# Optimization experiments

Measured on AMD Instinct MI355X. Metric: run time of the kernel, lower is better.

## Reference

```python
import jax, jax.numpy as jnp
import numpy as np

EMBED_DIM = 768
NUM_HEADS = 12
HEAD_DIM = EMBED_DIM // NUM_HEADS
SCALE = HEAD_DIM ** -0.5


def setup_inputs() -> dict:
    key = jax.random.key(0)
    ks = jax.random.split(key, 5)
    B, N, D = 2, 4096, EMBED_DIM
    std = 1.0 / np.sqrt(D)
    x = jax.random.normal(ks[0], (B, N, D), dtype=jnp.float32)
    W_qkv = jax.random.normal(ks[1], (D, 3 * D), dtype=jnp.float32) * std
    b_qkv = jax.random.normal(ks[2], (3 * D,), dtype=jnp.float32) * 0.01
    W_proj = jax.random.normal(ks[3], (D, D), dtype=jnp.float32) * std
    b_proj = jax.random.normal(ks[4], (D,), dtype=jnp.float32) * 0.01
    return {"x": x, "W_qkv": W_qkv, "b_qkv": b_qkv, "W_proj": W_proj, "b_proj": b_proj}


def reference(x, W_qkv, b_qkv, W_proj, b_proj):
    B, N, D = x.shape
    H, Hd = NUM_HEADS, HEAD_DIM
    qkv = x @ W_qkv + b_qkv                      # [B, N, 3D]
    qkv = qkv.reshape(B, N, 3, H, Hd)
    qkv = jnp.transpose(qkv, (2, 0, 3, 1, 4))    # [3, B, H, N, Hd]
    q, k, v = qkv[0], qkv[1], qkv[2]
    attn = jnp.einsum('bhqd,bhkd->bhqk', q, k) * SCALE   # [B, H, N, N]
    attn = jax.nn.softmax(attn, axis=-1)
    out = jnp.einsum('bhqk,bhkd->bhqd', attn, v)          # [B, H, N, Hd]
    out = jnp.transpose(out, (0, 2, 1, 3)).reshape(B, N, D)
    return out @ W_proj + b_proj
```

## Files before the change

### kernel.cpp

```cpp
#include <hip/hip_runtime.h>
#include <hip/hip_bf16.h>

typedef __attribute__((ext_vector_type(4))) float f32x4;
typedef __attribute__((ext_vector_type(16))) float f32x16;
typedef __attribute__((ext_vector_type(8))) short s16x8;
typedef __attribute__((ext_vector_type(4))) unsigned int u32x4;

#define MFMA16(a, b, c) __builtin_amdgcn_mfma_f32_16x16x32_bf16(a, b, c, 0, 0, 0)
#define MFMA32(a, b, c) __builtin_amdgcn_mfma_f32_32x32x16_bf16(a, b, c, 0, 0, 0)

__device__ __forceinline__ short f2bf(float f) {
  unsigned u = __builtin_bit_cast(unsigned, f);
  u += 0x7fffu + ((u >> 16) & 1u);
  return (short)(u >> 16);
}
__device__ __forceinline__ unsigned cvtpk(float lo, float hi) {
  unsigned r;
  asm("v_cvt_pk_bf16_f32 %0, %1, %2" : "=v"(r) : "v"(lo), "v"(hi));
  return r;
}
__device__ __forceinline__ float ex2(float x) {
  float r;
  asm("v_exp_f32 %0, %1" : "=v"(r) : "v"(x));
  return r;
}
__device__ __forceinline__ void vperm(const s16x8 a, const s16x8 b,
                                      s16x8& w0, s16x8& w1) {
#pragma unroll
  for (int e = 0; e < 4; ++e) {
    w0[e] = a[e];
    w0[4 + e] = b[e];
    w1[e] = a[4 + e];
    w1[4 + e] = b[4 + e];
  }
}
__device__ __forceinline__ void gl_lds16(const unsigned short* g, short* l) {
  __builtin_amdgcn_global_load_lds(
      (const __attribute__((address_space(1))) unsigned int*)g,
      (__attribute__((address_space(3))) unsigned int*)l, 16, 0, 0);
}

__global__ __launch_bounds__(256) void convert_x(
    const float* __restrict__ X, unsigned short* __restrict__ Xb) {
  const size_t i = ((size_t)blockIdx.x * 256 + threadIdx.x) * 8;
  f32x4 a = *(const f32x4*)(X + i);
  f32x4 b = *(const f32x4*)(X + i + 4);
  s16x8 o;
#pragma unroll
  for (int e = 0; e < 4; ++e) o[e] = f2bf(a[e]);
#pragma unroll
  for (int e = 0; e < 4; ++e) o[4 + e] = f2bf(b[e]);
  *(s16x8*)(Xb + i) = o;
}

__global__ __launch_bounds__(256) void tconv(
    const float* __restrict__ W, unsigned short* __restrict__ Wt,
    int K, int N) {
  __shared__ float T[64][65];
  const int k0 = blockIdx.x * 64, n0 = blockIdx.y * 64;
  const int t = threadIdx.x;
  const int tr = t >> 4, tc = (t & 15) * 4;
#pragma unroll
  for (int i = 0; i < 4; ++i) {
    f32x4 v = *(const f32x4*)&W[(size_t)(k0 + tr + i * 16) * N + n0 + tc];
#pragma unroll
    for (int e = 0; e < 4; ++e) T[tc + e][tr + i * 16] = v[e];
  }
  __syncthreads();
  const int nn = t >> 2, kk = (t & 3) * 16;
  s16x8 o0, o1;
#pragma unroll
  for (int j = 0; j < 8; ++j) o0[j] = f2bf(T[nn][kk + j]);
#pragma unroll
  for (int j = 0; j < 8; ++j) o1[j] = f2bf(T[nn][kk + 8 + j]);
  *(s16x8*)&Wt[(size_t)(n0 + nn) * K + k0 + kk] = o0;
  *(s16x8*)&Wt[(size_t)(n0 + nn) * K + k0 + kk + 8] = o1;
}

__global__ __launch_bounds__(256) void qkv_gemm(
    const unsigned short* __restrict__ Xb, const unsigned short* __restrict__ Wt,
    const float* __restrict__ bias, unsigned short* __restrict__ Qo,
    unsigned short* __restrict__ Ko, unsigned short* __restrict__ VTo) {
  __shared__ __align__(16) short As[128 * 32];
  __shared__ __align__(16) short Bs[128 * 32];
  const int m0 = blockIdx.x * 128, n0 = blockIdx.y * 128;
  const int tid = threadIdx.x, lane = tid & 63, wid = tid >> 6;
  const int wr = wid >> 1, wc = wid & 1;
  const int lr = lane & 15, s4 = lane >> 4;

  const int crow = lane >> 2;
  const int ccol = (lane & 3) ^ (crow & 3);
  const unsigned short* ga0 = Xb + (size_t)(m0 + wid * 32 + crow) * 768 + ccol * 8;
  const unsigned short* ga1 = ga0 + (size_t)16 * 768;
  const unsigned short* gb0 = Wt + (size_t)(n0 + wid * 32 + crow) * 768 + ccol * 8;
  const unsigned short* gb1 = gb0 + (size_t)16 * 768;
  short* lA0 = &As[(wid * 2) * 512];
  short* lA1 = &As[(wid * 2 + 1) * 512];
  short* lB0 = &Bs[(wid * 2) * 512];
  short* lB1 = &Bs[(wid * 2 + 1) * 512];

  f32x4 acc[4][4];
#pragma unroll
  for (int i = 0; i < 4; ++i)
#pragma unroll
    for (int j = 0; j < 4; ++j)
#pragma unroll
      for (int e = 0; e < 4; ++e) acc[i][j][e] = 0.f;

  for (int k0 = 0; k0 < 768; k0 += 32) {
    gl_lds16(ga0 + k0, lA0);
    gl_lds16(ga1 + k0, lA1);
    gl_lds16(gb0 + k0, lB0);
    gl_lds16(gb1 + k0, lB1);
    __syncthreads();
    s16x8 af[4], bfr[4];
#pragma unroll
    for (int mi = 0; mi < 4; ++mi) {
      const int row = wr * 64 + mi * 16 + lr;
      af[mi] = *(const s16x8*)&As[row * 32 + ((s4 ^ (row & 3)) << 3)];
    }
#pragma unroll
    for (int ni = 0; ni < 4; ++ni) {
      const int row = wc * 64 + ni * 16 + lr;
      bfr[ni] = *(const s16x8*)&Bs[row * 32 + ((s4 ^ (row & 3)) << 3)];
    }
#pragma unroll
    for (int mi = 0; mi < 4; ++mi)
#pragma unroll
      for (int ni = 0; ni < 4; ++ni)
        acc[mi][ni] = MFMA16(af[mi], bfr[ni], acc[mi][ni]);
    __syncthreads();
  }

  const float QSC = 0.18033688011f;
  const int rbase = m0 + wr * 64 + (lane >> 4) * 4;
#pragma unroll
  for (int ni = 0; ni < 4; ++ni) {
    const int cb = n0 + wc * 64 + ni * 16;
    const int which = cb / 768;
    const int rem = cb - which * 768;
    const int h = rem >> 6;
    const int d = (rem & 63) + lr;
    const float bi = bias[cb + lr];
#pragma unroll
    for (int mi = 0; mi < 4; ++mi) {
#pragma unroll
      for (int j = 0; j < 4; ++j) {
        const int row = rbase + mi * 16 + j;
        const int bb = row >> 12, t = row & 4095;
        const float v = acc[mi][ni][j] + bi;
        const size_t hb = (size_t)(bb * 12 + h);
        if (which == 0)
          Qo[(hb * 4096 + t) * 64 + d] = (unsigned short)f2bf(v * QSC);
        else if (which == 1)
          Ko[(hb * 4096 + t) * 64 + d] = (unsigned short)f2bf(v);
        else
          VTo[(hb * 64 + d) * 4096 + t] = (unsigned short)f2bf(v);
      }
    }
  }
}

__global__ __launch_bounds__(256) void attn_fwd(
    const unsigned short* __restrict__ Qg, const unsigned short* __restrict__ Kg,
    const unsigned short* __restrict__ VTg, unsigned short* __restrict__ Aout) {
  __shared__ __align__(16) short smem[16384];
  const int qt = blockIdx.x, bh = blockIdx.y;
  const unsigned short* Qh = Qg + (size_t)bh * 4096 * 64;
  const unsigned short* Kh = Kg + (size_t)bh * 4096 * 64;
  const unsigned short* Vh = VTg + (size_t)bh * 4096 * 64;
  const int tid = threadIdx.x, lane = tid & 63, wid = tid >> 6;
  const int l31 = lane & 31, hi = lane >> 5;
  const int sw0 = (l31 + (l31 >> 3)) & 7;
  const int sw1 = (sw0 + 4) & 7;
  const int qbase = qt * 128 + wid * 32;

  s16x8 qf[4];
#pragma unroll
  for (int db = 0; db < 4; ++db)
    qf[db] = *(const s16x8*)&Qh[(size_t)(qbase + l31) * 64 + db * 16 + hi * 8];

  s16x8 ones;
#pragma unroll
  for (int e = 0; e < 8; ++e) ones[e] = (short)0x3F80;

  f32x16 zf;
#pragma unroll
  for (int r = 0; r < 16; ++r) zf[r] = 0.f;
  f32x16 o0 = zf, o1 = zf, accl = zf;

  const int srow = tid >> 2, sp = tid & 3;
  const int ssw = (srow + (srow >> 3)) & 7;
  const int sd0 = srow * 64 + (((sp * 2) ^ ssw) << 3);
  const int sd1 = srow * 64 + (((sp * 2 + 1) ^ ssw) << 3);
  const unsigned short* kga = Kh + srow * 64 + sp * 16;
  const unsigned short* vga = Vh + (size_t)srow * 4096 + sp * 16;

  s16x8 kr0 = *(const s16x8*)kga;
  s16x8 kr1 = *(const s16x8*)(kga + 8);
  s16x8 vr0 = *(const s16x8*)vga;
  s16x8 vr1 = *(const s16x8*)(vga + 8);
  {
    s16x8 w0, w1;
    vperm(vr0, vr1, w0, w1);
    *(s16x8*)&smem[sd0] = kr0;
    *(s16x8*)&smem[sd1] = kr1;
    *(s16x8*)&smem[8192 + sd0] = w0;
    *(s16x8*)&smem[8192 + sd1] = w1;
  }
  __syncthreads();

  int cur = 0;
  for (int t = 0; t < 64; ++t) {
    if (t < 63) {
      kr0 = *(const s16x8*)(kga + (size_t)(t + 1) * 4096);
      kr1 = *(const s16x8*)(kga + (size_t)(t + 1) * 4096 + 8);
      vr0 = *(const s16x8*)(vga + (t + 1) * 64);
      vr1 = *(const s16x8*)(vga + (t + 1) * 64 + 8);
    }
    const short* Kc = smem + cur * 4096;
    const short* Vc = smem + 8192 + cur * 4096;

    f32x16 sA = zf, sB = zf;
    __builtin_amdgcn_s_setprio(1);
#pragma unroll
    for (int db = 0; db < 4; ++db) {
      s16x8 kf = *(const s16x8*)&Kc[l31 * 64 + (((db * 2 + hi) ^ sw0) << 3)];
      sA = MFMA32(kf, qf[db], sA);
    }
#pragma unroll
    for (int db = 0; db < 4; ++db) {
      s16x8 kf = *(const s16x8*)&Kc[(32 + l31) * 64 + (((db * 2 + hi) ^ sw1) << 3)];
      sB = MFMA32(kf, qf[db], sB);
    }
    __builtin_amdgcn_s_setprio(0);

#pragma unroll
    for (int r = 0; r < 16; ++r) {
      sA[r] = ex2(sA[r]);
      sB[r] = ex2(sB[r]);
    }
    s16x8 pf0, pf1, pf2, pf3;
#define PACK_PF(pfv, sv, bse)                                           \
  {                                                                     \
    u32x4 fw;                                                           \
    fw[0] = cvtpk(sv[bse + 0], sv[bse + 1]);                            \
    fw[1] = cvtpk(sv[bse + 2], sv[bse + 3]);                            \
    fw[2] = cvtpk(sv[bse + 4], sv[bse + 5]);                            \
    fw[3] = cvtpk(sv[bse + 6], sv[bse + 7]);                            \
    pfv = __builtin_bit_cast(s16x8, fw);                                \
  }
    PACK_PF(pf0, sA, 0)
    PACK_PF(pf1, sA, 8)
    PACK_PF(pf2, sB, 0)
    PACK_PF(pf3, sB, 8)
#undef PACK_PF

    __builtin_amdgcn_s_setprio(1);
    accl = MFMA32(ones, pf0, accl);
    accl = MFMA32(ones, pf1, accl);
    accl = MFMA32(ones, pf2, accl);
    accl = MFMA32(ones, pf3, accl);

    {
      const short* Vr = &Vc[l31 * 64];
      s16x8 v0 = *(const s16x8*)&Vr[((0 + hi) ^ sw0) << 3];
      o0 = MFMA32(v0, pf0, o0);
      s16x8 v1 = *(const s16x8*)&Vr[((2 + hi) ^ sw0) << 3];
      o0 = MFMA32(v1, pf1, o0);
      s16x8 v2 = *(const s16x8*)&Vr[((4 + hi) ^ sw0) << 3];
      o0 = MFMA32(v2, pf2, o0);
      s16x8 v3 = *(const s16x8*)&Vr[((6 + hi) ^ sw0) << 3];
      o0 = MFMA32(v3, pf3, o0);
      const short* Vr1 = &Vc[(32 + l31) * 64];
      s16x8 w0 = *(const s16x8*)&Vr1[((0 + hi) ^ sw1) << 3];
      o1 = MFMA32(w0, pf0, o1);
      s16x8 w1 = *(const s16x8*)&Vr1[((2 + hi) ^ sw1) << 3];
      o1 = MFMA32(w1, pf1, o1);
      s16x8 w2 = *(const s16x8*)&Vr1[((4 + hi) ^ sw1) << 3];
      o1 = MFMA32(w2, pf2, o1);
      s16x8 w3 = *(const s16x8*)&Vr1[((6 + hi) ^ sw1) << 3];
      o1 = MFMA32(w3, pf3, o1);
    }
    __builtin_amdgcn_s_setprio(0);

    if (t < 63) {
      const int nb = cur ^ 1;
      s16x8 w0, w1;
      vperm(vr0, vr1, w0, w1);
      *(s16x8*)&smem[nb * 4096 + sd0] = kr0;
      *(s16x8*)&smem[nb * 4096 + sd1] = kr1;
      *(s16x8*)&smem[8192 + nb * 4096 + sd0] = w0;
      *(s16x8*)&smem[8192 + nb * 4096 + sd1] = w1;
      __syncthreads();
      cur = nb;
    }
  }

  __syncthreads();
  short* Ow = smem + wid * (32 * 72);
  const float inv = 1.0f / accl[0];
#pragma unroll
  for (int r = 0; r < 16; ++r) {
    const int dd = (r & 3) + 8 * (r >> 2) + 4 * hi;
    Ow[l31 * 72 + dd] = f2bf(o0[r] * inv);
    Ow[l31 * 72 + 32 + dd] = f2bf(o1[r] * inv);
  }
  const int b = bh / 12, h = bh - b * 12;
  const int qq = lane >> 1, c0 = (lane & 1) * 32;
  const size_t gb = ((size_t)(b * 4096 + qbase + qq)) * 768 + h * 64 + c0;
#pragma unroll
  for (int i = 0; i < 4; ++i) {
    s16x8 v = *(const s16x8*)&Ow[qq * 72 + c0 + i * 8];
    *(s16x8*)&Aout[gb + i * 8] = v;
  }
}

__global__ __launch_bounds__(256) void proj_gemm(
    const unsigned short* __restrict__ A, const unsigned short* __restrict__ Wt,
    const float* __restrict__ bias, float* __restrict__ out) {
  __shared__ __align__(16) short As[128 * 32];
  __shared__ __align__(16) short Bs[128 * 32];
  const int m0 = blockIdx.x * 128, n0 = blockIdx.y * 128;
  const int tid = threadIdx.x, lane = tid & 63, wid = tid >> 6;
  const int wr = wid >> 1, wc = wid & 1;
  const int lr = lane & 15, s4 = lane >> 4;

  const int crow = lane >> 2;
  const int ccol = (lane & 3) ^ (crow & 3);
  const unsigned short* ga0 = A + (size_t)(m0 + wid * 32 + crow) * 768 + ccol * 8;
  const unsigned short* ga1 = ga0 + (size_t)16 * 768;
  const unsigned short* gb0 = Wt + (size_t)(n0 + wid * 32 + crow) * 768 + ccol * 8;
  const unsigned short* gb1 = gb0 + (size_t)16 * 768;
  short* lA0 = &As[(wid * 2) * 512];
  short* lA1 = &As[(wid * 2 + 1) * 512];
  short* lB0 = &Bs[(wid * 2) * 512];
  short* lB1 = &Bs[(wid * 2 + 1) * 512];

  f32x4 acc[4][4];
#pragma unroll
  for (int i = 0; i < 4; ++i)
#pragma unroll
    for (int j = 0; j < 4; ++j)
#pragma unroll
      for (int e = 0; e < 4; ++e) acc[i][j][e] = 0.f;

  for (int k0 = 0; k0 < 768; k0 += 32) {
    gl_lds16(ga0 + k0, lA0);
    gl_lds16(ga1 + k0, lA1);
    gl_lds16(gb0 + k0, lB0);
    gl_lds16(gb1 + k0, lB1);
    __syncthreads();
    s16x8 af[4], bfr[4];
#pragma unroll
    for (int mi = 0; mi < 4; ++mi) {
      const int row = wr * 64 + mi * 16 + lr;
      af[mi] = *(const s16x8*)&As[row * 32 + ((s4 ^ (row & 3)) << 3)];
    }
#pragma unroll
    for (int ni = 0; ni < 4; ++ni) {
      const int row = wc * 64 + ni * 16 + lr;
      bfr[ni] = *(const s16x8*)&Bs[row * 32 + ((s4 ^ (row & 3)) << 3)];
    }
#pragma unroll
    for (int mi = 0; mi < 4; ++mi)
#pragma unroll
      for (int ni = 0; ni < 4; ++ni)
        acc[mi][ni] = MFMA16(af[mi], bfr[ni], acc[mi][ni]);
    __syncthreads();
  }

  const int rbase = m0 + wr * 64 + (lane >> 4) * 4;
#pragma unroll
  for (int ni = 0; ni < 4; ++ni) {
    const int cb = n0 + wc * 64 + ni * 16;
    const float bi = bias[cb + lr];
#pragma unroll
    for (int mi = 0; mi < 4; ++mi) {
#pragma unroll
      for (int j = 0; j < 4; ++j) {
        const int row = rbase + mi * 16 + j;
        out[(size_t)row * 768 + cb + lr] = acc[mi][ni][j] + bi;
      }
    }
  }
}

extern "C" void kernel_launch(void* const* d_in, const int* in_sizes, int n_in,
                              void* d_out, int out_size, void* d_ws, size_t ws_size,
                              hipStream_t stream) {
  const float* x = (const float*)d_in[0];
  const float* W_qkv = (const float*)d_in[1];
  const float* b_qkv = (const float*)d_in[2];
  const float* W_proj = (const float*)d_in[3];
  const float* b_proj = (const float*)d_in[4];
  float* out = (float*)d_out;

  unsigned short* ws = (unsigned short*)d_ws;
  const size_t NQ = (size_t)24 * 4096 * 64;
  unsigned short* q = ws;
  unsigned short* k = ws + NQ;
  unsigned short* vt = ws + 2 * NQ;
  unsigned short* xb_attn = ws + 3 * NQ;
  unsigned short* wqt = ws + 4 * NQ;
  unsigned short* wpt = wqt + (size_t)2304 * 768;

  convert_x<<<3072, 256, 0, stream>>>(x, xb_attn);
  tconv<<<dim3(12, 36), 256, 0, stream>>>(W_qkv, wqt, 768, 2304);
  tconv<<<dim3(12, 12), 256, 0, stream>>>(W_proj, wpt, 768, 768);
  qkv_gemm<<<dim3(64, 18), 256, 0, stream>>>(xb_attn, wqt, b_qkv, q, k, vt);
  attn_fwd<<<dim3(32, 24), 256, 0, stream>>>(q, k, vt, xb_attn);
  proj_gemm<<<dim3(64, 6), 256, 0, stream>>>(xb_attn, wpt, b_proj, out);
}
```

Measured before the change: 233.3 us.

## Split attention KV range in two and combine partial outputs

```diff
diff --git a/kernel.cpp b/kernel.cpp
--- a/kernel.cpp
+++ b/kernel.cpp
@@ -161,11 +161,15 @@
   }
 }
 
+template <int NSPLIT>
 __global__ __launch_bounds__(256) void attn_fwd(
     const unsigned short* __restrict__ Qg, const unsigned short* __restrict__ Kg,
-    const unsigned short* __restrict__ VTg, unsigned short* __restrict__ Aout) {
+    const unsigned short* __restrict__ VTg, unsigned short* __restrict__ Aout,
+    float* __restrict__ Opart, float* __restrict__ Lpart) {
+  constexpr int TKV = 64 / NSPLIT;
   __shared__ __align__(16) short smem[16384];
-  const int qt = blockIdx.x, bh = blockIdx.y;
+  const int qt = blockIdx.x, bh = blockIdx.y, sz = blockIdx.z;
+  const int tok0 = sz * TKV * 64;
   const unsigned short* Qh = Qg + (size_t)bh * 4096 * 64;
   const unsigned short* Kh = Kg + (size_t)bh * 4096 * 64;
   const unsigned short* Vh = VTg + (size_t)bh * 4096 * 64;
@@ -193,8 +197,8 @@
   const int ssw = (srow + (srow >> 3)) & 7;
   const int sd0 = srow * 64 + (((sp * 2) ^ ssw) << 3);
   const int sd1 = srow * 64 + (((sp * 2 + 1) ^ ssw) << 3);
-  const unsigned short* kga = Kh + srow * 64 + sp * 16;
-  const unsigned short* vga = Vh + (size_t)srow * 4096 + sp * 16;
+  const unsigned short* kga = Kh + (size_t)(tok0 + srow) * 64 + sp * 16;
+  const unsigned short* vga = Vh + (size_t)srow * 4096 + tok0 + sp * 16;
 
   s16x8 kr0 = *(const s16x8*)kga;
   s16x8 kr1 = *(const s16x8*)(kga + 8);
@@ -211,8 +215,8 @@
   __syncthreads();
 
   int cur = 0;
-  for (int t = 0; t < 64; ++t) {
-    if (t < 63) {
+  for (int t = 0; t < TKV; ++t) {
+    if (t < TKV - 1) {
       kr0 = *(const s16x8*)(kga + (size_t)(t + 1) * 4096);
       kr1 = *(const s16x8*)(kga + (size_t)(t + 1) * 4096 + 8);
       vr0 = *(const s16x8*)(vga + (t + 1) * 64);
@@ -284,7 +288,7 @@
     }
     __builtin_amdgcn_s_setprio(0);
 
-    if (t < 63) {
+    if (t < TKV - 1) {
       const int nb = cur ^ 1;
       s16x8 w0, w1;
       vperm(vr0, vr1, w0, w1);
@@ -297,23 +301,67 @@
     }
   }
 
+  if constexpr (NSPLIT == 1) {
+    __syncthreads();
+    short* Ow = smem + wid * (32 * 72);
+    const float inv = 1.0f / accl[0];
+#pragma unroll
+    for (int r = 0; r < 16; ++r) {
+      const int dd = (r & 3) + 8 * (r >> 2) + 4 * hi;
+      Ow[l31 * 72 + dd] = f2bf(o0[r] * inv);
+      Ow[l31 * 72 + 32 + dd] = f2bf(o1[r] * inv);
+    }
+    const int b = bh / 12, h = bh - b * 12;
+    const int qq = lane >> 1, c0 = (lane & 1) * 32;
+    const size_t gb = ((size_t)(b * 4096 + qbase + qq)) * 768 + h * 64 + c0;
+#pragma unroll
+    for (int i = 0; i < 4; ++i) {
+      s16x8 v = *(const s16x8*)&Ow[qq * 72 + c0 + i * 8];
+      *(s16x8*)&Aout[gb + i * 8] = v;
+    }
+  } else {
+    const int q = qbase + l31;
+    const size_t ob = ((size_t)(sz * 24 + bh)) * 64 * 4096;
+#pragma unroll
+    for (int r = 0; r < 16; ++r) {
+      const int dd = (r & 3) + 8 * (r >> 2) + 4 * hi;
+      Opart[ob + (size_t)dd * 4096 + q] = o0[r];
+      Opart[ob + (size_t)(dd + 32) * 4096 + q] = o1[r];
+    }
+    Lpart[(size_t)(sz * 24 + bh) * 4096 + q] = accl[0];
+  }
+}
+
+__global__ __launch_bounds__(256) void attn_combine(
+    const float* __restrict__ Opart, const float* __restrict__ Lpart,
+    unsigned short* __restrict__ Aout) {
+  __shared__ float T[64][65];
+  const int q0 = blockIdx.x * 64, bh = blockIdx.y;
+  const int t = threadIdx.x;
+  const int d = t >> 2, qc = (t & 3) * 16;
+  const size_t b0 = ((size_t)bh * 64 + d) * 4096 + q0 + qc;
+  const size_t b1 = ((size_t)(24 + bh) * 64 + d) * 4096 + q0 + qc;
+#pragma unroll
+  for (int i = 0; i < 4; ++i) {
+    f32x4 v = *(const f32x4*)&Opart[b0 + i * 4];
+    f32x4 w = *(const f32x4*)&Opart[b1 + i * 4];
+#pragma unroll
+    for (int e = 0; e < 4; ++e) T[qc + i * 4 + e][d] = v[e] + w[e];
+  }
   __syncthreads();
-  short* Ow = smem + wid * (32 * 72);
-  const float inv = 1.0f / accl[0];
-#pragma unroll
-  for (int r = 0; r < 16; ++r) {
-    const int dd = (r & 3) + 8 * (r >> 2) + 4 * hi;
-    Ow[l31 * 72 + dd] = f2bf(o0[r] * inv);
-    Ow[l31 * 72 + 32 + dd] = f2bf(o1[r] * inv);
-  }
+  const int q = t >> 2, dc = (t & 3) * 16;
+  const float l = Lpart[(size_t)bh * 4096 + q0 + q] +
+                  Lpart[(size_t)(24 + bh) * 4096 + q0 + q];
+  const float inv = 1.0f / l;
   const int b = bh / 12, h = bh - b * 12;
-  const int qq = lane >> 1, c0 = (lane & 1) * 32;
-  const size_t gb = ((size_t)(b * 4096 + qbase + qq)) * 768 + h * 64 + c0;
-#pragma unroll
-  for (int i = 0; i < 4; ++i) {
-    s16x8 v = *(const s16x8*)&Ow[qq * 72 + c0 + i * 8];
-    *(s16x8*)&Aout[gb + i * 8] = v;
-  }
+  s16x8 o0, o1;
+#pragma unroll
+  for (int e = 0; e < 8; ++e) o0[e] = f2bf(T[q][dc + e] * inv);
+#pragma unroll
+  for (int e = 0; e < 8; ++e) o1[e] = f2bf(T[q][dc + 8 + e] * inv);
+  const size_t gb = ((size_t)(b * 4096 + q0 + q)) * 768 + h * 64 + dc;
+  *(s16x8*)&Aout[gb] = o0;
+  *(s16x8*)&Aout[gb + 8] = o1;
 }
 
 __global__ __launch_bounds__(256) void proj_gemm(
@@ -405,10 +453,22 @@
   unsigned short* wqt = ws + 4 * NQ;
   unsigned short* wpt = wqt + (size_t)2304 * 768;
 
+  const size_t base_bytes = (4 * NQ + (size_t)2304 * 768 + (size_t)768 * 768) * 2;
+  const size_t opart_bytes = (size_t)2 * 24 * 64 * 4096 * 4;
+  const size_t lpart_bytes = (size_t)2 * 24 * 4096 * 4;
+  const bool split = ws_size >= base_bytes + opart_bytes + lpart_bytes;
+  float* Opart = (float*)((char*)d_ws + base_bytes);
+  float* Lpart = (float*)((char*)d_ws + base_bytes + opart_bytes);
+
   convert_x<<<3072, 256, 0, stream>>>(x, xb_attn);
   tconv<<<dim3(12, 36), 256, 0, stream>>>(W_qkv, wqt, 768, 2304);
   tconv<<<dim3(12, 12), 256, 0, stream>>>(W_proj, wpt, 768, 768);
   qkv_gemm<<<dim3(64, 18), 256, 0, stream>>>(xb_attn, wqt, b_qkv, q, k, vt);
-  attn_fwd<<<dim3(32, 24), 256, 0, stream>>>(q, k, vt, xb_attn);
+  if (split) {
+    attn_fwd<2><<<dim3(32, 24, 2), 256, 0, stream>>>(q, k, vt, xb_attn, Opart, Lpart);
+    attn_combine<<<dim3(64, 24), 256, 0, stream>>>(Opart, Lpart, xb_attn);
+  } else {
+    attn_fwd<1><<<dim3(32, 24, 1), 256, 0, stream>>>(q, k, vt, xb_attn, Opart, Lpart);
+  }
   proj_gemm<<<dim3(64, 6), 256, 0, stream>>>(xb_attn, wpt, b_proj, out);
 }
```

After: 242.2 us. 3.8% more time.

## Load K/V tiles directly to LDS and pre-permute V^T in QKV epilogue

Applied to the files above, without the earlier changes.

```diff
diff --git a/kernel.cpp b/kernel.cpp
--- a/kernel.cpp
+++ b/kernel.cpp
@@ -23,16 +23,6 @@
   float r;
   asm("v_exp_f32 %0, %1" : "=v"(r) : "v"(x));
   return r;
-}
-__device__ __forceinline__ void vperm(const s16x8 a, const s16x8 b,
-                                      s16x8& w0, s16x8& w1) {
-#pragma unroll
-  for (int e = 0; e < 4; ++e) {
-    w0[e] = a[e];
-    w0[4 + e] = b[e];
-    w1[e] = a[4 + e];
-    w1[4 + e] = b[4 + e];
-  }
 }
 __device__ __forceinline__ void gl_lds16(const unsigned short* g, short* l) {
   __builtin_amdgcn_global_load_lds(
@@ -133,7 +123,9 @@
   }
 
   const float QSC = 0.18033688011f;
-  const int rbase = m0 + wr * 64 + (lane >> 4) * 4;
+  const int lg = lane >> 4;
+  const int plg = ((lg & 1) << 1) | ((lg >> 1) & 1);
+  const int rbase = m0 + wr * 64 + lg * 4;
 #pragma unroll
   for (int ni = 0; ni < 4; ++ni) {
     const int cb = n0 + wc * 64 + ni * 16;
@@ -154,8 +146,10 @@
           Qo[(hb * 4096 + t) * 64 + d] = (unsigned short)f2bf(v * QSC);
         else if (which == 1)
           Ko[(hb * 4096 + t) * 64 + d] = (unsigned short)f2bf(v);
-        else
-          VTo[(hb * 64 + d) * 4096 + t] = (unsigned short)f2bf(v);
+        else {
+          const int tp = (t & ~15) + plg * 4 + j;
+          VTo[(hb * 64 + d) * 4096 + tp] = (unsigned short)f2bf(v);
+        }
       }
     }
   }
@@ -189,34 +183,34 @@
   for (int r = 0; r < 16; ++r) zf[r] = 0.f;
   f32x16 o0 = zf, o1 = zf, accl = zf;
 
-  const int srow = tid >> 2, sp = tid & 3;
-  const int ssw = (srow + (srow >> 3)) & 7;
-  const int sd0 = srow * 64 + (((sp * 2) ^ ssw) << 3);
-  const int sd1 = srow * 64 + (((sp * 2 + 1) ^ ssw) << 3);
-  const unsigned short* kga = Kh + srow * 64 + sp * 16;
-  const unsigned short* vga = Vh + (size_t)srow * 4096 + sp * 16;
-
-  s16x8 kr0 = *(const s16x8*)kga;
-  s16x8 kr1 = *(const s16x8*)(kga + 8);
-  s16x8 vr0 = *(const s16x8*)vga;
-  s16x8 vr1 = *(const s16x8*)(vga + 8);
-  {
-    s16x8 w0, w1;
-    vperm(vr0, vr1, w0, w1);
-    *(s16x8*)&smem[sd0] = kr0;
-    *(s16x8*)&smem[sd1] = kr1;
-    *(s16x8*)&smem[8192 + sd0] = w0;
-    *(s16x8*)&smem[8192 + sd1] = w1;
-  }
+  const int r0 = wid * 16 + (lane >> 3);
+  const int r1 = r0 + 8;
+  const int c16 = lane & 7;
+  const int sc0 = (c16 ^ ((r0 + (r0 >> 3)) & 7)) << 3;
+  const int sc1 = (c16 ^ ((r1 + (r1 >> 3)) & 7)) << 3;
+  const unsigned short* kg0 = Kh + (size_t)r0 * 64 + sc0;
+  const unsigned short* kg1 = Kh + (size_t)r1 * 64 + sc1;
+  const unsigned short* vg0 = Vh + (size_t)r0 * 4096 + sc0;
+  const unsigned short* vg1 = Vh + (size_t)r1 * 4096 + sc1;
+  short* const ldsK0 = &smem[(wid * 2) * 512];
+  short* const ldsK1 = &smem[(wid * 2 + 1) * 512];
+  short* const ldsV0 = &smem[8192 + (wid * 2) * 512];
+  short* const ldsV1 = &smem[8192 + (wid * 2 + 1) * 512];
+
+  gl_lds16(kg0, ldsK0);
+  gl_lds16(kg1, ldsK1);
+  gl_lds16(vg0, ldsV0);
+  gl_lds16(vg1, ldsV1);
   __syncthreads();
 
   int cur = 0;
   for (int t = 0; t < 64; ++t) {
     if (t < 63) {
-      kr0 = *(const s16x8*)(kga + (size_t)(t + 1) * 4096);
-      kr1 = *(const s16x8*)(kga + (size_t)(t + 1) * 4096 + 8);
-      vr0 = *(const s16x8*)(vga + (t + 1) * 64);
-      vr1 = *(const s16x8*)(vga + (t + 1) * 64 + 8);
+      const int nb = (cur ^ 1) * 4096;
+      gl_lds16(kg0 + (size_t)(t + 1) * 4096, ldsK0 + nb);
+      gl_lds16(kg1 + (size_t)(t + 1) * 4096, ldsK1 + nb);
+      gl_lds16(vg0 + (t + 1) * 64, ldsV0 + nb);
+      gl_lds16(vg1 + (t + 1) * 64, ldsV1 + nb);
     }
     const short* Kc = smem + cur * 4096;
     const short* Vc = smem + 8192 + cur * 4096;
@@ -285,15 +279,8 @@
     __builtin_amdgcn_s_setprio(0);
 
     if (t < 63) {
-      const int nb = cur ^ 1;
-      s16x8 w0, w1;
-      vperm(vr0, vr1, w0, w1);
-      *(s16x8*)&smem[nb * 4096 + sd0] = kr0;
-      *(s16x8*)&smem[nb * 4096 + sd1] = kr1;
-      *(s16x8*)&smem[8192 + nb * 4096 + sd0] = w0;
-      *(s16x8*)&smem[8192 + nb * 4096 + sd1] = w1;
       __syncthreads();
-      cur = nb;
+      cur ^= 1;
     }
   }
 
```

Result: slower. 243.8 us (+4.5%).
